# Performance work log

Measured on AMD Instinct MI355X. Metric: run time of the kernel, lower is better.

The kernel has to match this reference:

```python
import jax, jax.numpy as jnp
import numpy as np

B, L, H = 256, 2048, 64

def _min_gru(x, Wz, bz, Wh, bh):
    # x: [B, L, Din] -> h: [B, L, H] via parallel scan of h_t = (1-z_t)*h_{t-1} + z_t*h~_t, h_0 = 0
    z = jax.nn.sigmoid(jnp.einsum('bli,ih->blh', x, Wz) + bz)
    h_tilde = jnp.einsum('bli,ih->blh', x, Wh) + bh
    a = 1.0 - z
    b = z * h_tilde
    def combine(c1, c2):
        a1, b1 = c1
        a2, b2 = c2
        return a1 * a2, b1 * a2 + b2
    _, h = jax.lax.associative_scan(combine, (a, b), axis=1)
    return h

def _stacked(x, Wz0, bz0, Wh0, bh0, Wz1, bz1, Wh1, bh1, Wo, bo):
    h = _min_gru(x, Wz0, bz0, Wh0, bh0)
    h = _min_gru(h, Wz1, bz1, Wh1, bh1)
    return jnp.einsum('blh,ho->blo', h, Wo) + bo  # [B, L, 1]

def setup_inputs():
    key = jax.random.key(0)
    ks = jax.random.split(key, 32)
    inputs = jax.random.bernoulli(ks[0], 0.5, (B, L)).astype(jnp.float32)
    p_array = jax.random.permutation(ks[1], L).astype(jnp.int32)
    def lin(k, fin, fout):
        return (jax.random.normal(k, (fin, fout), jnp.float32) / np.float32(np.sqrt(fin)))
    d = {'inputs': inputs, 'p_array': p_array}
    i = 2
    for r in (1, 2):
        for nm, fin, fout in (('z0', 1, H), ('h0', 1, H), ('z1', H, H), ('h1', H, H), ('o', H, 1)):
            d['w%d%s' % (r, nm)] = lin(ks[i], fin, fout); i += 1
            d['b%d%s' % (r, nm)] = jnp.zeros((fout,), jnp.float32)
    return d

def reference(inputs, p_array, w1z0, b1z0, w1h0, b1h0, w1z1, b1z1, w1h1, b1h1, w1o, b1o,
              w2z0, b2z0, w2h0, b2h0, w2z1, b2z1, w2h1, b2h1, w2o, b2o):
    x = inputs[..., None]                      # [B, L, 1]
    x_sys = _stacked(x, w1z0, b1z0, w1h0, b1h0, w1z1, b1z1, w1h1, b1h1, w1o, b1o)
    x_int = x[:, p_array, :]                   # interleave along sequence dim
    x_p1 = _stacked(x_int, w2z0, b2z0, w2h0, b2h0, w2z1, b2z1, w2h1, b2h1, w2o, b2o)
    x_tx = jnp.concatenate([x_sys, x_p1], axis=2)  # [B, L, 2]
    mean = jnp.mean(x_tx)
    std = jnp.std(x_tx, ddof=1)                # torch.std is unbiased by default
    return (x_tx - mean) / std                 # squeeze(dim=2) is a no-op on size-2 dim
```

## Files before the change

kernel.cpp:

```cpp
#include <hip/hip_runtime.h>

#define BB 256
#define LL 2048
#define HH 64
#define TT 64
#define SS 68
#define NCH (LL / TT)
#define NTOT (BB * LL * 2)

typedef __attribute__((ext_vector_type(8))) short bf16x8;
typedef __attribute__((ext_vector_type(4))) float f32x4;

__device__ __forceinline__ float rcp_(float x) { return __builtin_amdgcn_rcpf(x); }

__device__ __forceinline__ short f2bf_rne(float f) {
    union { float f; unsigned u; } v; v.f = f;
    unsigned r = v.u + 0x7fff + ((v.u >> 16) & 1);
    return (short)(r >> 16);
}

template<int CTRL>
__device__ __forceinline__ float qdpp(float x) {
    union { float f; int i; } u, r;
    u.f = x;
    r.i = __builtin_amdgcn_update_dpp(0, u.i, CTRL, 0xF, 0xF, false);
    return r.f;
}

template<int D>
__device__ __forceinline__ float rshr(float x) {
    union { float f; int i; } u, r;
    u.f = x;
    r.i = __builtin_amdgcn_update_dpp(0, u.i, 0x110 | D, 0xF, 0xF, true);
    return r.f;
}

__device__ __forceinline__ void p1_scan(const float* __restrict__ sxp,
                                        float a0v, float b0v, float a1v, float b1v,
                                        int seg, int col0, float& carry, float* sh)
{
    float xi[16];
    #pragma unroll
    for (int k = 0; k < 4; ++k) {
        const float4 v = *(const float4*)(sxp + 4 * k);
        xi[4*k+0] = v.x; xi[4*k+1] = v.y; xi[4*k+2] = v.z; xi[4*k+3] = v.w;
    }
    float ai[16], bi[16];
    float A = 1.0f, Bv = 0.0f;
    #pragma unroll
    for (int i = 0; i < 16; ++i) {
        const bool on = (xi[i] != 0.0f);
        ai[i] = on ? a1v : a0v;
        bi[i] = on ? b1v : b0v;
        A  = A * ai[i];
        Bv = fmaf(Bv, ai[i], bi[i]);
    }
    {
        const float Au = qdpp<0x90>(A), Bu = qdpp<0x90>(Bv);
        if (seg >= 1) { const float Ac = A; A = Au * Ac; Bv = fmaf(Bu, Ac, Bv); }
        const float Au2 = qdpp<0x44>(A), Bu2 = qdpp<0x44>(Bv);
        if (seg >= 2) { const float Ac = A; A = Au2 * Ac; Bv = fmaf(Bu2, Ac, Bv); }
    }
    float Ae = qdpp<0x90>(A), Be = qdpp<0x90>(Bv);
    if (seg == 0) { Ae = 1.0f; Be = 0.0f; }
    float cc = fmaf(Ae, carry, Be);
    #pragma unroll
    for (int i = 0; i < 16; ++i) {
        cc = fmaf(ai[i], cc, bi[i]);
        sh[(seg * 16 + i) * SS + col0] = cc;
    }
    carry = qdpp<0xFF>(cc);
}

__global__ void __launch_bounds__(256)
__attribute__((amdgpu_waves_per_eu(2, 2)))
gru_fused(const float* __restrict__ x, const int* __restrict__ p,
               const float* __restrict__ w1z0, const float* __restrict__ b1z0,
               const float* __restrict__ w1h0, const float* __restrict__ b1h0,
               const float* __restrict__ w1z1, const float* __restrict__ b1z1,
               const float* __restrict__ w1h1, const float* __restrict__ b1h1,
               const float* __restrict__ w1o,  const float* __restrict__ b1o,
               const float* __restrict__ w2z0, const float* __restrict__ b2z0,
               const float* __restrict__ w2h0, const float* __restrict__ b2h0,
               const float* __restrict__ w2z1, const float* __restrict__ b2z1,
               const float* __restrict__ w2h1, const float* __restrict__ b2h1,
               const float* __restrict__ w2o,  const float* __restrict__ b2o,
               float* __restrict__ out, float* __restrict__ ws)
{
    const int  b  = blockIdx.x;
    const bool pm = (blockIdx.y != 0);

    const float* wz0 = pm ? w2z0 : w1z0;
    const float* bz0 = pm ? b2z0 : b1z0;
    const float* wh0 = pm ? w2h0 : w1h0;
    const float* bh0 = pm ? b2h0 : b1h0;
    const float* wz1 = pm ? w2z1 : w1z1;
    const float* bz1 = pm ? b2z1 : b1z1;
    const float* wh1 = pm ? w2h1 : w1h1;
    const float* bh1 = pm ? b2h1 : b1h1;
    const float* wo  = pm ? w2o  : w1o;
    const float* bov = pm ? b2o  : b1o;

    const int tid  = threadIdx.x;
    const int lane = tid & 63;
    const int tg   = tid >> 6;
    const int q    = lane >> 4;
    const int n    = lane & 15;
    const int seg  = lane & 3;
    const int hidx = (tg << 4) | (lane >> 2);

    __shared__ __align__(16) float s_h[2 * TT * SS];
    __shared__ __align__(16) float s_x[LL];
    __shared__ float2 s_w[2][4][HH];
    __shared__ float s_red[8];

    const float* xrow = x + (size_t)b * LL;

    if (!pm) {
        const float4* x4 = (const float4*)xrow;
        float4* sx4 = (float4*)s_x;
        #pragma unroll
        for (int i = 0; i < LL / 4 / 256; ++i)
            sx4[tid + 256 * i] = x4[tid + 256 * i];
    } else {
        const int4* p4 = (const int4*)p;
        float4* sx4 = (float4*)s_x;
        #pragma unroll
        for (int i = 0; i < LL / 4 / 256; ++i) {
            const int4 v = p4[tid + 256 * i];
            float4 w;
            w.x = xrow[v.x]; w.y = xrow[v.y]; w.z = xrow[v.z]; w.w = xrow[v.w];
            sx4[tid + 256 * i] = w;
        }
    }

    const float z0v = rcp_(1.0f + __expf(-bz0[hidx]));
    const float z1v = rcp_(1.0f + __expf(-(wz0[hidx] + bz0[hidx])));
    const float a0v = 1.0f - z0v, b0v = z0v * bh0[hidx];
    const float a1v = 1.0f - z1v, b1v = z1v * (wh0[hidx] + bh0[hidx]);

    float rbz1[4], rbh1[4], rwo4[4];
    #pragma unroll
    for (int ht = 0; ht < 4; ++ht) {
        rbz1[ht] = bz1[ht * 16 + n];
        rbh1[ht] = bh1[ht * 16 + n];
        rwo4[ht] = wo[ht * 16 + n];
    }
    const float bo = bov[0];

    bf16x8 wfz[2][4], wfh[2][4];
    for (int ks = 0; ks < 2; ++ks) {
        for (int ht = 0; ht < 4; ++ht) {
            #pragma unroll
            for (int j = 0; j < 8; ++j) {
                const int kk = ks * 32 + q * 8 + j;
                const int hh = ht * 16 + n;
                wfz[ks][ht][j] = f2bf_rne(wz1[kk * HH + hh]);
                wfh[ks][ht][j] = f2bf_rne(wh1[kk * HH + hh]);
            }
        }
    }

    float carry0 = 0.0f;
    float carry1[4] = {0.0f, 0.0f, 0.0f, 0.0f};
    f32x4 ga[4], gb[4];
    float Aqe[4], Bqe[4];
    float lsum = 0.0f, lsum2 = 0.0f;
    float* outp = out + (pm ? 1 : 0);
    const int t0 = tg * 16;
    const int col0 = hidx ^ ((seg & 1) << 4);

    auto g2_step = [&](int cm) {
        const int buf = cm & 1;
        float Acm[4] = {1,1,1,1}, Bcm[4] = {0,0,0,0};
        float Ap[4], Bp[4];
        #pragma unroll
        for (int w = 0; w < 4; ++w) {
            #pragma unroll
            for (int ht = 0; ht < 4; ++ht) {
                if (w == tg) { Ap[ht] = Acm[ht]; Bp[ht] = Bcm[ht]; }
                const float2 ab = s_w[buf][w][ht * 16 + n];
                Bcm[ht] = fmaf(ab.x, Bcm[ht], ab.y);
                Acm[ht] *= ab.x;
            }
        }
        float vo[4] = {0,0,0,0};
        #pragma unroll
        for (int ht = 0; ht < 4; ++ht) {
            float cc = fmaf(Aqe[ht], fmaf(Ap[ht], carry1[ht], Bp[ht]), Bqe[ht]);
            #pragma unroll
            for (int r = 0; r < 4; ++r) {
                cc = fmaf(ga[ht][r], cc, gb[ht][r]);
                vo[r] = fmaf(cc, rwo4[ht], vo[r]);
            }
            carry1[ht] = fmaf(Acm[ht], carry1[ht], Bcm[ht]);
        }
        #pragma unroll
        for (int r = 0; r < 4; ++r) {
            vo[r] += rshr<1>(vo[r]);
            vo[r] += rshr<2>(vo[r]);
            vo[r] += rshr<4>(vo[r]);
            vo[r] += rshr<8>(vo[r]);
        }
        if (n == 15) {
            #pragma unroll
            for (int r = 0; r < 4; ++r) {
                const float v = vo[r] + bo;
                outp[((size_t)b * LL + cm * TT + t0 + q * 4 + r) * 2] = v;
                lsum += v;
                lsum2 = fmaf(v, v, lsum2);
            }
        }
    };

    __syncthreads();

    p1_scan(s_x + seg * 16, a0v, b0v, a1v, b1v, seg, col0, carry0, s_h);
    __syncthreads();

    for (int c = 0; c < NCH; ++c) {
        const int cp1 = c + 1;

        if (c > 0) g2_step(c - 1);

        {
            #pragma unroll
            for (int ht = 0; ht < 4; ++ht) {
                ga[ht] = (f32x4){rbz1[ht], rbz1[ht], rbz1[ht], rbz1[ht]};
                gb[ht] = (f32x4){rbh1[ht], rbh1[ht], rbh1[ht], rbh1[ht]};
            }
            const float* shR = s_h + (c & 1) * (TT * SS);
            const int qs = q ^ ((tg & 1) << 1);
            #pragma unroll
            for (int ks = 0; ks < 2; ++ks) {
                const float* ap = &shR[(t0 + n) * SS + ks * 32 + qs * 8];
                const float4 av0 = *(const float4*)ap;
                const float4 av1 = *(const float4*)(ap + 4);
                float af[8] = {av0.x, av0.y, av0.z, av0.w, av1.x, av1.y, av1.z, av1.w};
                bf16x8 ahi, alo;
                #pragma unroll
                for (int j = 0; j < 8; ++j) {
                    union { float f; unsigned u; } uf; uf.f = af[j];
                    ahi[j] = (short)(uf.u >> 16);
                    union { unsigned u; float f; } hf; hf.u = uf.u & 0xffff0000u;
                    const float rem = af[j] - hf.f;
                    union { float f; unsigned u; } ur; ur.f = rem;
                    alo[j] = (short)(ur.u >> 16);
                }
                #pragma unroll
                for (int ht = 0; ht < 4; ++ht) {
                    ga[ht] = __builtin_amdgcn_mfma_f32_16x16x32_bf16(ahi, wfz[ks][ht], ga[ht], 0, 0, 0);
                    ga[ht] = __builtin_amdgcn_mfma_f32_16x16x32_bf16(alo, wfz[ks][ht], ga[ht], 0, 0, 0);
                    gb[ht] = __builtin_amdgcn_mfma_f32_16x16x32_bf16(ahi, wfh[ks][ht], gb[ht], 0, 0, 0);
                    gb[ht] = __builtin_amdgcn_mfma_f32_16x16x32_bf16(alo, wfh[ks][ht], gb[ht], 0, 0, 0);
                }
            }
            #pragma unroll
            for (int ht = 0; ht < 4; ++ht) {
                #pragma unroll
                for (int r = 0; r < 4; ++r) {
                    const float v   = ga[ht][r];
                    const float a   = rcp_(1.0f + __expf(v));
                    const float htl = gb[ht][r];
                    ga[ht][r] = a;
                    gb[ht][r] = fmaf(-a, htl, htl);
                }
            }
            float Aq[4], Bq[4];
            #pragma unroll
            for (int ht = 0; ht < 4; ++ht) {
                float A = 1.0f, B = 0.0f;
                #pragma unroll
                for (int r = 0; r < 4; ++r) {
                    B = fmaf(ga[ht][r], B, gb[ht][r]);
                    A = A * ga[ht][r];
                }
                Aq[ht] = A; Bq[ht] = B;
            }
            #pragma unroll
            for (int ht = 0; ht < 4; ++ht) {
                const float Au = __shfl_up(Aq[ht], 16), Bu = __shfl_up(Bq[ht], 16);
                if (q >= 1) { const float Ac = Aq[ht]; Aq[ht] = Ac * Au; Bq[ht] = fmaf(Ac, Bu, Bq[ht]); }
            }
            #pragma unroll
            for (int ht = 0; ht < 4; ++ht) {
                const float Au = __shfl_up(Aq[ht], 32), Bu = __shfl_up(Bq[ht], 32);
                if (q >= 2) { const float Ac = Aq[ht]; Aq[ht] = Ac * Au; Bq[ht] = fmaf(Ac, Bu, Bq[ht]); }
            }
            #pragma unroll
            for (int ht = 0; ht < 4; ++ht) {
                const float Ae = __shfl_up(Aq[ht], 16), Be = __shfl_up(Bq[ht], 16);
                Aqe[ht] = (q == 0) ? 1.0f : Ae;
                Bqe[ht] = (q == 0) ? 0.0f : Be;
            }
            if (q == 3) {
                #pragma unroll
                for (int ht = 0; ht < 4; ++ht)
                    s_w[c & 1][tg][ht * 16 + n] = make_float2(Aq[ht], Bq[ht]);
            }
        }

        if (cp1 < NCH)
            p1_scan(s_x + cp1 * TT + seg * 16, a0v, b0v, a1v, b1v, seg, col0, carry0,
                    s_h + (cp1 & 1) * (TT * SS));

        __syncthreads();
    }

    g2_step(NCH - 1);

    #pragma unroll
    for (int o = 32; o; o >>= 1) {
        lsum  += __shfl_down(lsum, o);
        lsum2 += __shfl_down(lsum2, o);
    }
    if (lane == 0) { s_red[tg] = lsum; s_red[4 + tg] = lsum2; }
    __syncthreads();
    if (tid == 0) {
        const int gb2 = b * 2 + (pm ? 1 : 0);
        ws[2 * gb2]     = s_red[0] + s_red[1] + s_red[2] + s_red[3];
        ws[2 * gb2 + 1] = s_red[4] + s_red[5] + s_red[6] + s_red[7];
    }
}

__global__ void normalize_k(float* __restrict__ out, const float* __restrict__ ws)
{
    __shared__ float s_red[8];
    float s = 0.0f, s2 = 0.0f;
    for (int i = threadIdx.x; i < 2 * BB; i += 256) {
        s  += ws[2 * i];
        s2 += ws[2 * i + 1];
    }
    #pragma unroll
    for (int o = 32; o; o >>= 1) {
        s  += __shfl_down(s, o);
        s2 += __shfl_down(s2, o);
    }
    const int wid = threadIdx.x >> 6;
    if ((threadIdx.x & 63) == 0) { s_red[wid] = s; s_red[4 + wid] = s2; }
    __syncthreads();
    const float tot  = s_red[0] + s_red[1] + s_red[2] + s_red[3];
    const float tot2 = s_red[4] + s_red[5] + s_red[6] + s_red[7];
    const float N    = (float)NTOT;
    const float mean = tot / N;
    const float var  = (tot2 - N * mean * mean) / (N - 1.0f);
    const float inv  = rsqrtf(var);

    const int i = blockIdx.x * blockDim.x + threadIdx.x;
    float4* o4 = (float4*)out;
    float4 v = o4[i];
    v.x = (v.x - mean) * inv;
    v.y = (v.y - mean) * inv;
    v.z = (v.z - mean) * inv;
    v.w = (v.w - mean) * inv;
    o4[i] = v;
}

extern "C" void kernel_launch(void* const* d_in, const int* in_sizes, int n_in,
                              void* d_out, int out_size, void* d_ws, size_t ws_size,
                              hipStream_t stream)
{
    (void)in_sizes; (void)n_in; (void)out_size; (void)ws_size;
    const float* x = (const float*)d_in[0];
    const int*   p = (const int*)d_in[1];
    float* out = (float*)d_out;
    float* ws  = (float*)d_ws;

    dim3 grid(BB, 2);
    gru_fused<<<grid, 256, 0, stream>>>(
        x, p,
        (const float*)d_in[2],  (const float*)d_in[3],
        (const float*)d_in[4],  (const float*)d_in[5],
        (const float*)d_in[6],  (const float*)d_in[7],
        (const float*)d_in[8],  (const float*)d_in[9],
        (const float*)d_in[10], (const float*)d_in[11],
        (const float*)d_in[12], (const float*)d_in[13],
        (const float*)d_in[14], (const float*)d_in[15],
        (const float*)d_in[16], (const float*)d_in[17],
        (const float*)d_in[18], (const float*)d_in[19],
        (const float*)d_in[20], (const float*)d_in[21],
        out, ws);

    normalize_k<<<NTOT / 4 / 256, 256, 0, stream>>>(out, ws);
}
```

Baseline: 187.7 us.

## Double chunk size to 128 with 512-thread blocks and bit-packed input

```diff
diff --git a/kernel.cpp b/kernel.cpp
--- a/kernel.cpp
+++ b/kernel.cpp
@@ -3,7 +3,7 @@
 #define BB 256
 #define LL 2048
 #define HH 64
-#define TT 64
+#define TT 128
 #define SS 68
 #define NCH (LL / TT)
 #define NTOT (BB * LL * 2)
@@ -17,14 +17,6 @@
     union { float f; unsigned u; } v; v.f = f;
     unsigned r = v.u + 0x7fff + ((v.u >> 16) & 1);
     return (short)(r >> 16);
-}
-
-template<int CTRL>
-__device__ __forceinline__ float qdpp(float x) {
-    union { float f; int i; } u, r;
-    u.f = x;
-    r.i = __builtin_amdgcn_update_dpp(0, u.i, CTRL, 0xF, 0xF, false);
-    return r.f;
 }
 
 template<int D>
@@ -35,33 +27,35 @@
     return r.f;
 }
 
-__device__ __forceinline__ void p1_scan(const float* __restrict__ sxp,
+__device__ __forceinline__ void p1_scan(const unsigned* __restrict__ bw, int c,
                                         float a0v, float b0v, float a1v, float b1v,
-                                        int seg, int col0, float& carry, float* sh)
+                                        int seg, int col0, int lane7,
+                                        float& carry, float* sh)
 {
-    float xi[16];
-    #pragma unroll
-    for (int k = 0; k < 4; ++k) {
-        const float4 v = *(const float4*)(sxp + 4 * k);
-        xi[4*k+0] = v.x; xi[4*k+1] = v.y; xi[4*k+2] = v.z; xi[4*k+3] = v.w;
-    }
+    const unsigned bits = (bw[c * 4 + (seg >> 1)] >> ((seg & 1) << 4)) & 0xffffu;
     float ai[16], bi[16];
     float A = 1.0f, Bv = 0.0f;
     #pragma unroll
     for (int i = 0; i < 16; ++i) {
-        const bool on = (xi[i] != 0.0f);
+        const bool on = (bits >> i) & 1u;
         ai[i] = on ? a1v : a0v;
         bi[i] = on ? b1v : b0v;
         A  = A * ai[i];
         Bv = fmaf(Bv, ai[i], bi[i]);
     }
     {
-        const float Au = qdpp<0x90>(A), Bu = qdpp<0x90>(Bv);
+        const float Au = rshr<1>(A), Bu = rshr<1>(Bv);
         if (seg >= 1) { const float Ac = A; A = Au * Ac; Bv = fmaf(Bu, Ac, Bv); }
-        const float Au2 = qdpp<0x44>(A), Bu2 = qdpp<0x44>(Bv);
-        if (seg >= 2) { const float Ac = A; A = Au2 * Ac; Bv = fmaf(Bu2, Ac, Bv); }
-    }
-    float Ae = qdpp<0x90>(A), Be = qdpp<0x90>(Bv);
+    }
+    {
+        const float Au = rshr<2>(A), Bu = rshr<2>(Bv);
+        if (seg >= 2) { const float Ac = A; A = Au * Ac; Bv = fmaf(Bu, Ac, Bv); }
+    }
+    {
+        const float Au = rshr<4>(A), Bu = rshr<4>(Bv);
+        if (seg >= 4) { const float Ac = A; A = Au * Ac; Bv = fmaf(Bu, Ac, Bv); }
+    }
+    float Ae = rshr<1>(A), Be = rshr<1>(Bv);
     if (seg == 0) { Ae = 1.0f; Be = 0.0f; }
     float cc = fmaf(Ae, carry, Be);
     #pragma unroll
@@ -69,11 +63,11 @@
         cc = fmaf(ai[i], cc, bi[i]);
         sh[(seg * 16 + i) * SS + col0] = cc;
     }
-    carry = qdpp<0xFF>(cc);
-}
-
-__global__ void __launch_bounds__(256)
-__attribute__((amdgpu_waves_per_eu(2, 2)))
+    carry = __shfl(cc, lane7);
+}
+
+__global__ void __launch_bounds__(512)
+__attribute__((amdgpu_waves_per_eu(4, 4)))
 gru_fused(const float* __restrict__ x, const int* __restrict__ p,
                const float* __restrict__ w1z0, const float* __restrict__ b1z0,
                const float* __restrict__ w1h0, const float* __restrict__ b1h0,
@@ -101,38 +95,30 @@
     const float* wo  = pm ? w2o  : w1o;
     const float* bov = pm ? b2o  : b1o;
 
-    const int tid  = threadIdx.x;
-    const int lane = tid & 63;
-    const int tg   = tid >> 6;
-    const int q    = lane >> 4;
-    const int n    = lane & 15;
-    const int seg  = lane & 3;
-    const int hidx = (tg << 4) | (lane >> 2);
+    const int tid   = threadIdx.x;
+    const int lane  = tid & 63;
+    const int tg    = tid >> 6;
+    const int q     = lane >> 4;
+    const int n     = lane & 15;
+    const int seg   = lane & 7;
+    const int hidx  = (tg << 3) | (lane >> 3);
+    const int lane7 = lane | 7;
 
     __shared__ __align__(16) float s_h[2 * TT * SS];
-    __shared__ __align__(16) float s_x[LL];
-    __shared__ float2 s_w[2][4][HH];
-    __shared__ float s_red[8];
+    __shared__ unsigned long long s_xb[LL / 64];
+    __shared__ float2 s_w[2][8][HH];
+    __shared__ float s_red[16];
 
     const float* xrow = x + (size_t)b * LL;
 
-    if (!pm) {
-        const float4* x4 = (const float4*)xrow;
-        float4* sx4 = (float4*)s_x;
-        #pragma unroll
-        for (int i = 0; i < LL / 4 / 256; ++i)
-            sx4[tid + 256 * i] = x4[tid + 256 * i];
-    } else {
-        const int4* p4 = (const int4*)p;
-        float4* sx4 = (float4*)s_x;
-        #pragma unroll
-        for (int i = 0; i < LL / 4 / 256; ++i) {
-            const int4 v = p4[tid + 256 * i];
-            float4 w;
-            w.x = xrow[v.x]; w.y = xrow[v.y]; w.z = xrow[v.z]; w.w = xrow[v.w];
-            sx4[tid + 256 * i] = w;
-        }
-    }
+    #pragma unroll
+    for (int g = 0; g < 4; ++g) {
+        const int idx = tg * 256 + g * 64 + lane;
+        const int src = pm ? p[idx] : idx;
+        const unsigned long long m = __ballot(xrow[src] != 0.0f);
+        if (lane == 0) s_xb[tg * 4 + g] = m;
+    }
+    const unsigned* bw = (const unsigned*)s_xb;
 
     const float z0v = rcp_(1.0f + __expf(-bz0[hidx]));
     const float z1v = rcp_(1.0f + __expf(-(wz0[hidx] + bz0[hidx])));
@@ -168,14 +154,14 @@
     float lsum = 0.0f, lsum2 = 0.0f;
     float* outp = out + (pm ? 1 : 0);
     const int t0 = tg * 16;
-    const int col0 = hidx ^ ((seg & 1) << 4);
+    const int col0 = hidx ^ ((seg & 1) << 4) ^ ((seg & 2) << 2);
 
     auto g2_step = [&](int cm) {
         const int buf = cm & 1;
         float Acm[4] = {1,1,1,1}, Bcm[4] = {0,0,0,0};
         float Ap[4], Bp[4];
         #pragma unroll
-        for (int w = 0; w < 4; ++w) {
+        for (int w = 0; w < 8; ++w) {
             #pragma unroll
             for (int ht = 0; ht < 4; ++ht) {
                 if (w == tg) { Ap[ht] = Acm[ht]; Bp[ht] = Bcm[ht]; }
@@ -215,7 +201,7 @@
 
     __syncthreads();
 
-    p1_scan(s_x + seg * 16, a0v, b0v, a1v, b1v, seg, col0, carry0, s_h);
+    p1_scan(bw, 0, a0v, b0v, a1v, b1v, seg, col0, lane7, carry0, s_h);
     __syncthreads();
 
     for (int c = 0; c < NCH; ++c) {
@@ -230,7 +216,7 @@
                 gb[ht] = (f32x4){rbh1[ht], rbh1[ht], rbh1[ht], rbh1[ht]};
             }
             const float* shR = s_h + (c & 1) * (TT * SS);
-            const int qs = q ^ ((tg & 1) << 1);
+            const int qs = q ^ (((tg & 1) << 1) | ((tg >> 1) & 1));
             #pragma unroll
             for (int ks = 0; ks < 2; ++ks) {
                 const float* ap = &shR[(t0 + n) * SS + ks * 32 + qs * 8];
@@ -301,7 +287,7 @@
         }
 
         if (cp1 < NCH)
-            p1_scan(s_x + cp1 * TT + seg * 16, a0v, b0v, a1v, b1v, seg, col0, carry0,
+            p1_scan(bw, cp1, a0v, b0v, a1v, b1v, seg, col0, lane7, carry0,
                     s_h + (cp1 & 1) * (TT * SS));
 
         __syncthreads();
@@ -314,12 +300,15 @@
         lsum  += __shfl_down(lsum, o);
         lsum2 += __shfl_down(lsum2, o);
     }
-    if (lane == 0) { s_red[tg] = lsum; s_red[4 + tg] = lsum2; }
+    if (lane == 0) { s_red[tg] = lsum; s_red[8 + tg] = lsum2; }
     __syncthreads();
     if (tid == 0) {
+        float s = 0.0f, s2 = 0.0f;
+        #pragma unroll
+        for (int i = 0; i < 8; ++i) { s += s_red[i]; s2 += s_red[8 + i]; }
         const int gb2 = b * 2 + (pm ? 1 : 0);
-        ws[2 * gb2]     = s_red[0] + s_red[1] + s_red[2] + s_red[3];
-        ws[2 * gb2 + 1] = s_red[4] + s_red[5] + s_red[6] + s_red[7];
+        ws[2 * gb2]     = s;
+        ws[2 * gb2 + 1] = s2;
     }
 }
 
@@ -367,7 +356,7 @@
     float* ws  = (float*)d_ws;
 
     dim3 grid(BB, 2);
-    gru_fused<<<grid, 256, 0, stream>>>(
+    gru_fused<<<grid, 512, 0, stream>>>(
         x, p,
         (const float*)d_in[2],  (const float*)d_in[3],
         (const float*)d_in[4],  (const float*)d_in[5],
```

After: 382.4 us. 104% more time.

## Bit-pack binary inputs via ballot and raise waves-per-EU target

Applied to the files above, without the earlier changes.

```diff
diff --git a/kernel.cpp b/kernel.cpp
--- a/kernel.cpp
+++ b/kernel.cpp
@@ -35,25 +35,19 @@
     return r.f;
 }
 
-__device__ __forceinline__ void p1_scan(const float* __restrict__ sxp,
+__device__ __forceinline__ void p1_scan(const unsigned* __restrict__ bw, int c,
                                         float a0v, float b0v, float a1v, float b1v,
                                         int seg, int col0, float& carry, float* sh)
 {
-    float xi[16];
-    #pragma unroll
-    for (int k = 0; k < 4; ++k) {
-        const float4 v = *(const float4*)(sxp + 4 * k);
-        xi[4*k+0] = v.x; xi[4*k+1] = v.y; xi[4*k+2] = v.z; xi[4*k+3] = v.w;
-    }
-    float ai[16], bi[16];
+    const unsigned bits = (bw[c * 2 + (seg >> 1)] >> ((seg & 1) << 4)) & 0xffffu;
     float A = 1.0f, Bv = 0.0f;
     #pragma unroll
     for (int i = 0; i < 16; ++i) {
-        const bool on = (xi[i] != 0.0f);
-        ai[i] = on ? a1v : a0v;
-        bi[i] = on ? b1v : b0v;
-        A  = A * ai[i];
-        Bv = fmaf(Bv, ai[i], bi[i]);
+        const bool on = (bits >> i) & 1u;
+        const float a = on ? a1v : a0v;
+        const float b = on ? b1v : b0v;
+        A  = A * a;
+        Bv = fmaf(Bv, a, b);
     }
     {
         const float Au = qdpp<0x90>(A), Bu = qdpp<0x90>(Bv);
@@ -66,14 +60,17 @@
     float cc = fmaf(Ae, carry, Be);
     #pragma unroll
     for (int i = 0; i < 16; ++i) {
-        cc = fmaf(ai[i], cc, bi[i]);
+        const bool on = (bits >> i) & 1u;
+        const float a = on ? a1v : a0v;
+        const float b = on ? b1v : b0v;
+        cc = fmaf(a, cc, b);
         sh[(seg * 16 + i) * SS + col0] = cc;
     }
     carry = qdpp<0xFF>(cc);
 }
 
 __global__ void __launch_bounds__(256)
-__attribute__((amdgpu_waves_per_eu(2, 2)))
+__attribute__((amdgpu_waves_per_eu(3, 4)))
 gru_fused(const float* __restrict__ x, const int* __restrict__ p,
                const float* __restrict__ w1z0, const float* __restrict__ b1z0,
                const float* __restrict__ w1h0, const float* __restrict__ b1h0,
@@ -110,29 +107,20 @@
     const int hidx = (tg << 4) | (lane >> 2);
 
     __shared__ __align__(16) float s_h[2 * TT * SS];
-    __shared__ __align__(16) float s_x[LL];
+    __shared__ unsigned long long s_xb[LL / 64];
     __shared__ float2 s_w[2][4][HH];
     __shared__ float s_red[8];
 
     const float* xrow = x + (size_t)b * LL;
 
-    if (!pm) {
-        const float4* x4 = (const float4*)xrow;
-        float4* sx4 = (float4*)s_x;
-        #pragma unroll
-        for (int i = 0; i < LL / 4 / 256; ++i)
-            sx4[tid + 256 * i] = x4[tid + 256 * i];
-    } else {
-        const int4* p4 = (const int4*)p;
-        float4* sx4 = (float4*)s_x;
-        #pragma unroll
-        for (int i = 0; i < LL / 4 / 256; ++i) {
-            const int4 v = p4[tid + 256 * i];
-            float4 w;
-            w.x = xrow[v.x]; w.y = xrow[v.y]; w.z = xrow[v.z]; w.w = xrow[v.w];
-            sx4[tid + 256 * i] = w;
-        }
-    }
+    #pragma unroll
+    for (int g = 0; g < 8; ++g) {
+        const int idx = g * 256 + tid;
+        const int src = pm ? p[idx] : idx;
+        const unsigned long long m = __ballot(xrow[src] != 0.0f);
+        if (lane == 0) s_xb[g * 4 + tg] = m;
+    }
+    const unsigned* bw = (const unsigned*)s_xb;
 
     const float z0v = rcp_(1.0f + __expf(-bz0[hidx]));
     const float z1v = rcp_(1.0f + __expf(-(wz0[hidx] + bz0[hidx])));
@@ -215,7 +203,7 @@
 
     __syncthreads();
 
-    p1_scan(s_x + seg * 16, a0v, b0v, a1v, b1v, seg, col0, carry0, s_h);
+    p1_scan(bw, 0, a0v, b0v, a1v, b1v, seg, col0, carry0, s_h);
     __syncthreads();
 
     for (int c = 0; c < NCH; ++c) {
@@ -301,7 +289,7 @@
         }
 
         if (cp1 < NCH)
-            p1_scan(s_x + cp1 * TT + seg * 16, a0v, b0v, a1v, b1v, seg, col0, carry0,
+            p1_scan(bw, cp1, a0v, b0v, a1v, b1v, seg, col0, carry0,
                     s_h + (cp1 & 1) * (TT * SS));
 
         __syncthreads();
```

After: 281.2 us. +49.8%, slower.
